# Performance work log

Hardware: AMD Instinct MI355X
Metric: run time of the kernel (lower is better)

Reference implementation:

```python
import jax, jax.numpy as jnp
import numpy as np

N = 50000   # nodes
E = 800000  # edges
IN, H, O, C = 128, 256, 256, 64
G = 64      # graphs in batch


def setup_inputs() -> dict:
    key = jax.random.key(0)
    ks = jax.random.split(key, 10)
    x = jax.random.normal(ks[0], (N, IN), dtype=jnp.float32)
    edge_index = jax.random.randint(ks[1], (2, E), 0, N, dtype=jnp.int32)
    batch = jnp.sort(jax.random.randint(ks[2], (N,), 0, G, dtype=jnp.int32))
    # learned params (PyG GCNConv: weight [in, out] + bias [out]; nn.Linear)
    W1 = jax.random.normal(ks[3], (IN, H), dtype=jnp.float32) / np.sqrt(IN)
    b1 = jnp.zeros((H,), dtype=jnp.float32)
    W2 = jax.random.normal(ks[4], (H, O), dtype=jnp.float32) / np.sqrt(H)
    b2 = jnp.zeros((O,), dtype=jnp.float32)
    Wfc = jax.random.normal(ks[5], (O, C), dtype=jnp.float32) / np.sqrt(O)
    bfc = jnp.zeros((C,), dtype=jnp.float32)
    return {"x": x, "edge_index": edge_index, "batch": batch,
            "W1": W1, "b1": b1, "W2": W2, "b2": b2, "Wfc": Wfc, "bfc": bfc}


def reference(x, edge_index, batch, W1, b1, W2, b2, Wfc, bfc):
    src, dst = edge_index[0], edge_index[1]
    # degree with self-loops (PyG GCNConv default: add_self_loops=True, sym norm)
    deg = jax.ops.segment_sum(jnp.ones((E,), x.dtype), dst, num_segments=N) + 1.0
    dinv = jax.lax.rsqrt(deg)                      # D^{-1/2}
    edge_norm = (dinv[src] * dinv[dst])[:, None]   # [E, 1]
    self_norm = (dinv * dinv)[:, None]             # [N, 1] self-loop weight

    def gcn_conv(h, W, b):
        h = h @ W                                  # transform first (PyG order)
        agg = jax.ops.segment_sum(h[src] * edge_norm, dst, num_segments=N)
        return agg + h * self_norm + b

    h = jax.nn.gelu(gcn_conv(x, W1, b1), approximate=False)  # nn.GELU exact
    h = gcn_conv(h, W2, b2)

    # global_mean_pool over graph ids
    cnt = jax.ops.segment_sum(jnp.ones((N,), h.dtype), batch, num_segments=G)
    pooled = jax.ops.segment_sum(h, batch, num_segments=G) / jnp.maximum(cnt, 1.0)[:, None]
    return pooled @ Wfc + bfc                      # [G, C]
```

## Files before the change

kernel.cpp:

```cpp
#include <hip/hip_runtime.h>
#include <hip/hip_bf16.h>
#include <hip/hip_fp16.h>
#include <math.h>

#define NNODES 50000
#define NEDGES 800000
#define FIN 128
#define FH 256
#define NG 64
#define NC 64
#define SCAN_NB ((NNODES + 255) / 256)
#define NP 50176
#define QSK 196
#define DEG_BLOCKS ((NEDGES + 255) / 256)
#define SPLITX_ITEMS (NNODES * FIN / 4)
#define SPLITX_BLOCKS ((SPLITX_ITEMS + 255) / 256)
#define WTZ_ITEMS (NG * NP / 4)
#define WTZ_BLOCKS ((WTZ_ITEMS + 255) / 256)
#define GEMM_MB ((NNODES + 127) / 128)
#define GEMM_BLKS (GEMM_MB * 2)
#define CVT_ITEMS (NG * NP / 4)
#define CVT_BLOCKS ((CVT_ITEMS + 255) / 256)

typedef unsigned short bhalf;
typedef __attribute__((ext_vector_type(8))) short bf16x8;
typedef __attribute__((ext_vector_type(4))) float f32x4;
typedef __attribute__((ext_vector_type(4))) unsigned short u16x4;

__device__ inline bhalf f2bf_rn(float f) {
    unsigned int u = __float_as_uint(f);
    u += 0x7FFFu + ((u >> 16) & 1u);
    return (bhalf)(u >> 16);
}
__device__ inline float bf2f(bhalf h) { return __uint_as_float(((unsigned int)h) << 16); }
__device__ inline float2 bfpair(unsigned int u) {
    return make_float2(__uint_as_float(u << 16), __uint_as_float(u & 0xFFFF0000u));
}
__device__ inline float edec_norm(unsigned int ed) {
    return __half2float(__ushort_as_half((unsigned short)(ed & 0xFFFFu)));
}


__global__ void degree_splitx_kernel(const int* __restrict__ dst, int* __restrict__ degi,
                                     int* __restrict__ rank, const float* __restrict__ x,
                                     bhalf* __restrict__ xb, float* __restrict__ wt) {
    int b = blockIdx.x;
    if (b < DEG_BLOCKS) {
        int e = b * 256 + threadIdx.x;
        if (e < NEDGES) rank[e] = atomicAdd(&degi[dst[e]], 1);
    } else if (b < DEG_BLOCKS + SPLITX_BLOCKS) {
        int i = (b - DEG_BLOCKS) * 256 + threadIdx.x;
        if (i < SPLITX_ITEMS) {
            float4 v = *reinterpret_cast<const float4*>(&x[i * 4]);
            u16x4 o = {f2bf_rn(v.x), f2bf_rn(v.y), f2bf_rn(v.z), f2bf_rn(v.w)};
            *reinterpret_cast<u16x4*>(&xb[i * 4]) = o;
        }
    } else {
        int i = (b - DEG_BLOCKS - SPLITX_BLOCKS) * 256 + threadIdx.x;
        if (i < WTZ_ITEMS) {
            f32x4 zr = {0.f, 0.f, 0.f, 0.f};
            *reinterpret_cast<f32x4*>(&wt[i * 4]) = zr;
        }
    }
}


__global__ __launch_bounds__(256)
void scan_block_kernel(const int* __restrict__ degi, int* __restrict__ local_ex,
                       int* __restrict__ partial, float* __restrict__ dinv, int Nn) {
    __shared__ int s[256];
    int i = blockIdx.x * 256 + threadIdx.x;
    int v = (i < Nn) ? degi[i] : 0;
    s[threadIdx.x] = v;
    __syncthreads();
#pragma unroll
    for (int off = 1; off < 256; off <<= 1) {
        int t = (threadIdx.x >= off) ? s[threadIdx.x - off] : 0;
        __syncthreads();
        s[threadIdx.x] += t;
        __syncthreads();
    }
    if (i < Nn) {
        local_ex[i] = s[threadIdx.x] - v;
        dinv[i] = rsqrtf((float)v + 1.0f);
    }
    if (threadIdx.x == 255) partial[blockIdx.x] = s[255];
}


__global__ __launch_bounds__(256)
void add_offsets_kernel(int* __restrict__ row_start, const int* __restrict__ local_ex,
                        const int* __restrict__ partial, const int* __restrict__ batch,
                        const float* __restrict__ dinv, float* __restrict__ wt,
                        const float* __restrict__ W1, bhalf* __restrict__ w1t, int Nn) {
    __shared__ int s[256];
    int t = threadIdx.x;
    s[t] = (t < blockIdx.x) ? partial[t] : 0;
    __syncthreads();
#pragma unroll
    for (int off = 128; off > 0; off >>= 1) {
        if (t < off) s[t] += s[t + off];
        __syncthreads();
    }
    int prefix = s[0];
    int i = blockIdx.x * 256 + t;
    if (i < Nn) {
        row_start[i] = local_ex[i] + prefix;
        float sn = dinv[i];
        atomicAdd(&wt[(size_t)batch[i] * NP + i], sn * sn);
    }
    if (i < FIN * 256) {
        int k = i >> 8, n = i & 255;
        w1t[n * FIN + k] = f2bf_rn(W1[i]);
    }
}


__global__ void edge_place_kernel(const int* __restrict__ src, const int* __restrict__ dst,
                                  const int* __restrict__ row_start, const int* __restrict__ rank,
                                  const float* __restrict__ dinv, const int* __restrict__ batch,
                                  unsigned int* __restrict__ edata, float* __restrict__ wt, int E) {
    int e = blockIdx.x * blockDim.x + threadIdx.x;
    if (e >= E) return;
    int s = src[e], d = dst[e];
    int pos = row_start[d] + rank[e];
    float nm = dinv[s] * dinv[d];
    unsigned short hb = __half_as_ushort(__float2half(nm));
    edata[pos] = ((unsigned int)s << 16) | (unsigned int)hb;
    atomicAdd(&wt[(size_t)batch[d] * NP + s], nm);
}


__global__ __launch_bounds__(256)
void gather128_kernel(const bhalf* __restrict__ xb, const unsigned int* __restrict__ edata,
                      const int* __restrict__ row_start, const int* __restrict__ degi,
                      const float* __restrict__ dinv, bhalf* __restrict__ z, int Nn) {
    int node = blockIdx.x * 4 + (threadIdx.x >> 6);
    if (node >= Nn) return;
    int lane = threadIdx.x & 63;
    int st = row_start[node];
    int cnt = degi[node];
    float ax = 0.0f, ay = 0.0f;
    int j = 0;
    for (; j + 3 < cnt; j += 4) {
        unsigned int e0 = edata[st + j],     e1 = edata[st + j + 1];
        unsigned int e2 = edata[st + j + 2], e3 = edata[st + j + 3];
        float2 v0 = bfpair(*reinterpret_cast<const unsigned int*>(&xb[(size_t)(e0 >> 16) * FIN + lane * 2]));
        float2 v1 = bfpair(*reinterpret_cast<const unsigned int*>(&xb[(size_t)(e1 >> 16) * FIN + lane * 2]));
        float2 v2 = bfpair(*reinterpret_cast<const unsigned int*>(&xb[(size_t)(e2 >> 16) * FIN + lane * 2]));
        float2 v3 = bfpair(*reinterpret_cast<const unsigned int*>(&xb[(size_t)(e3 >> 16) * FIN + lane * 2]));
        float n0 = edec_norm(e0), n1 = edec_norm(e1), n2 = edec_norm(e2), n3 = edec_norm(e3);
        ax += v0.x * n0 + v1.x * n1 + v2.x * n2 + v3.x * n3;
        ay += v0.y * n0 + v1.y * n1 + v2.y * n2 + v3.y * n3;
    }
    for (; j < cnt; j++) {
        unsigned int e0 = edata[st + j];
        float2 v0 = bfpair(*reinterpret_cast<const unsigned int*>(&xb[(size_t)(e0 >> 16) * FIN + lane * 2]));
        float n0 = edec_norm(e0);
        ax += v0.x * n0; ay += v0.y * n0;
    }
    float sn = dinv[node];
    sn *= sn;
    float2 xv = bfpair(*reinterpret_cast<const unsigned int*>(&xb[(size_t)node * FIN + lane * 2]));
    ushort2 o = {f2bf_rn(ax + xv.x * sn), f2bf_rn(ay + xv.y * sn)};
    *reinterpret_cast<ushort2*>(&z[(size_t)node * FIN + lane * 2]) = o;
}


__global__ __launch_bounds__(256)
void gemm_cvt_kernel(const bhalf* __restrict__ A, const bhalf* __restrict__ Bt,
                     const float* __restrict__ bias, bhalf* __restrict__ h1t,
                     const float* __restrict__ wt, bhalf* __restrict__ wthi,
                     bhalf* __restrict__ wtlo, int M, int Kp) {
    __shared__ bhalf As[128 * 72];
    __shared__ bhalf Bs[128 * 72];
    if (blockIdx.x >= GEMM_BLKS) {
        int i = (blockIdx.x - GEMM_BLKS) * 256 + threadIdx.x;
        if (i < CVT_ITEMS) {
            float4 v = *reinterpret_cast<const float4*>(&wt[i * 4]);
            u16x4 hi = {f2bf_rn(v.x), f2bf_rn(v.y), f2bf_rn(v.z), f2bf_rn(v.w)};
            u16x4 lo = {f2bf_rn(v.x - bf2f(hi.x)), f2bf_rn(v.y - bf2f(hi.y)),
                        f2bf_rn(v.z - bf2f(hi.z)), f2bf_rn(v.w - bf2f(hi.w))};
            *reinterpret_cast<u16x4*>(&wthi[i * 4]) = hi;
            *reinterpret_cast<u16x4*>(&wtlo[i * 4]) = lo;
        }
        return;
    }
    const int tid  = threadIdx.x;
    const int lane = tid & 63;
    const int wave = tid >> 6;
    const int quad = lane >> 4;
    const int l15  = lane & 15;
    const int wm = (wave & 1) * 64;
    const int wn = (wave >> 1) * 64;
    const int bm = (blockIdx.x >> 1) * 128;
    const int bn = (blockIdx.x & 1) * 128;

    f32x4 acc[4][4] = {};

    for (int k0 = 0; k0 < Kp; k0 += 64) {
#pragma unroll
        for (int i = 0; i < 4; i++) {
            int chunk = tid + i * 256;
            int r = chunk >> 3, c16 = chunk & 7;
            int gm = bm + r;
            float4 va = make_float4(0.f, 0.f, 0.f, 0.f);
            if (gm < M) va = *reinterpret_cast<const float4*>(&A[(size_t)gm * Kp + k0 + c16 * 8]);
            *reinterpret_cast<float4*>(&As[r * 72 + c16 * 8]) = va;
            float4 vb = *reinterpret_cast<const float4*>(&Bt[(size_t)(bn + r) * Kp + k0 + c16 * 8]);
            *reinterpret_cast<float4*>(&Bs[r * 72 + c16 * 8]) = vb;
        }
        __syncthreads();
#pragma unroll
        for (int kk = 0; kk < 64; kk += 32) {
            bf16x8 af[4], bfr[4];
#pragma unroll
            for (int mi = 0; mi < 4; mi++)
                af[mi] = *reinterpret_cast<const bf16x8*>(&As[(wm + mi * 16 + l15) * 72 + kk + quad * 8]);
#pragma unroll
            for (int ni = 0; ni < 4; ni++)
                bfr[ni] = *reinterpret_cast<const bf16x8*>(&Bs[(wn + ni * 16 + l15) * 72 + kk + quad * 8]);
#pragma unroll
            for (int mi = 0; mi < 4; mi++)
#pragma unroll
                for (int ni = 0; ni < 4; ni++)
                    acc[mi][ni] = __builtin_amdgcn_mfma_f32_16x16x32_bf16(af[mi], bfr[ni], acc[mi][ni], 0, 0, 0);
        }
        __syncthreads();
    }

#pragma unroll
    for (int mi = 0; mi < 4; mi++) {
        int row0 = bm + wm + mi * 16 + quad * 4;
#pragma unroll
        for (int ni = 0; ni < 4; ni++) {
            int col = bn + wn + ni * 16 + l15;
            float bv = bias[col];
            u16x4 o;
#pragma unroll
            for (int r = 0; r < 4; r++) {
                float v = acc[mi][ni][r] + bv;
                v = 0.5f * v * (1.0f + erff(v * 0.70710678118654752f));
                o[r] = f2bf_rn(v);
            }
            *reinterpret_cast<u16x4*>(&h1t[(size_t)col * NP + row0]) = o;
        }
    }
}


__global__ __launch_bounds__(256)
void qsum_mfma_kernel(const bhalf* __restrict__ h1t, const bhalf* __restrict__ wthi,
                      const bhalf* __restrict__ wtlo, float* __restrict__ qpart) {
    const int tid  = threadIdx.x;
    const int lane = tid & 63;
    const int wave = tid >> 6;
    const int quad = lane >> 4;
    const int l15  = lane & 15;
    const int m0 = wave * 64;
    const size_t kbase = (size_t)blockIdx.x * 256 + quad * 8;
    f32x4 acc[4][4] = {};
#pragma unroll
    for (int ks = 0; ks < 8; ks++) {
        size_t k0 = kbase + ks * 32;
        bf16x8 af[4], bh[4], bl[4];
#pragma unroll
        for (int mi = 0; mi < 4; mi++)
            af[mi] = *reinterpret_cast<const bf16x8*>(&h1t[(size_t)(m0 + mi * 16 + l15) * NP + k0]);
#pragma unroll
        for (int ni = 0; ni < 4; ni++) {
            bh[ni] = *reinterpret_cast<const bf16x8*>(&wthi[(size_t)(ni * 16 + l15) * NP + k0]);
            bl[ni] = *reinterpret_cast<const bf16x8*>(&wtlo[(size_t)(ni * 16 + l15) * NP + k0]);
        }
#pragma unroll
        for (int mi = 0; mi < 4; mi++)
#pragma unroll
            for (int ni = 0; ni < 4; ni++) {
                acc[mi][ni] = __builtin_amdgcn_mfma_f32_16x16x32_bf16(af[mi], bh[ni], acc[mi][ni], 0, 0, 0);
                acc[mi][ni] = __builtin_amdgcn_mfma_f32_16x16x32_bf16(af[mi], bl[ni], acc[mi][ni], 0, 0, 0);
            }
    }
    float* qp = &qpart[(size_t)blockIdx.x * NG * FH];
#pragma unroll
    for (int mi = 0; mi < 4; mi++) {
        int row0 = m0 + mi * 16 + quad * 4;
#pragma unroll
        for (int ni = 0; ni < 4; ni++) {
            int col = ni * 16 + l15;
            f32x4 o = {acc[mi][ni][0], acc[mi][ni][1], acc[mi][ni][2], acc[mi][ni][3]};
            *reinterpret_cast<f32x4*>(&qp[(size_t)col * FH + row0]) = o;
        }
    }
}


__global__ __launch_bounds__(256)
void p2fc_kernel(const float* __restrict__ qpart, const float* __restrict__ W2,
                 const float* __restrict__ b2, const int* __restrict__ batch,
                 const float* __restrict__ Wfc, const float* __restrict__ bfc,
                 float* __restrict__ out) {
    __shared__ float qg[FH];
    __shared__ float ps[FH];
    int g = blockIdx.x;
    int t = threadIdx.x;
    float s = 0.0f;
    for (int b = 0; b < QSK; b++)
        s += qpart[(size_t)b * NG * FH + (size_t)g * FH + t];
    qg[t] = s;
    int lo = 0, hi = NNODES;
    while (lo < hi) { int m = (lo + hi) >> 1; if (batch[m] < g) lo = m + 1; else hi = m; }
    int a = lo;
    lo = 0; hi = NNODES;
    while (lo < hi) { int m = (lo + hi) >> 1; if (batch[m] < g + 1) lo = m + 1; else hi = m; }
    float inv = 1.0f / fmaxf((float)(lo - a), 1.0f);
    __syncthreads();
    float acc = 0.0f;
    for (int k = 0; k < FH; k++)
        acc += qg[k] * W2[k * FH + t];
    ps[t] = acc * inv + b2[t];
    __syncthreads();
    if (t < NC) {
        float a2 = 0.0f;
        for (int cc = 0; cc < FH; cc++)
            a2 += ps[cc] * Wfc[cc * NC + t];
        out[g * NC + t] = a2 + bfc[t];
    }
}


extern "C" void kernel_launch(void* const* d_in, const int* in_sizes, int n_in,
                              void* d_out, int out_size, void* d_ws, size_t ws_size,
                              hipStream_t stream) {
    const float* x    = (const float*)d_in[0];
    const int*   ei   = (const int*)d_in[1];
    const int*   batch= (const int*)d_in[2];
    const float* W1   = (const float*)d_in[3];
    const float* b1   = (const float*)d_in[4];
    const float* W2   = (const float*)d_in[5];
    const float* b2   = (const float*)d_in[6];
    const float* Wfc  = (const float*)d_in[7];
    const float* bfc  = (const float*)d_in[8];
    float* out = (float*)d_out;

    const int* src = ei;
    const int* dst = ei + NEDGES;

    bhalf* xb        = (bhalf*)d_ws;
    bhalf* zb        = xb + (size_t)NNODES * FIN;
    bhalf* h1t       = zb + (size_t)NNODES * FIN;
    unsigned int* edata = (unsigned int*)(h1t + (size_t)FH * NP);
    int*   rank      = (int*)(edata + NEDGES);
    int*   row_start = rank + NEDGES;
    int*   local_ex  = row_start + NNODES;
    int*   partial   = local_ex + NNODES;
    float* dinv      = (float*)(partial + 256);
    bhalf* w1t       = (bhalf*)(dinv + NNODES);
    bhalf* wthi      = w1t + 256 * FIN;
    bhalf* wtlo      = wthi + (size_t)NG * NP;
    float* qpart     = (float*)(wtlo + (size_t)NG * NP);
    float* wt        = qpart + (size_t)QSK * NG * FH;
    int*   degi      = (int*)(wt + (size_t)NG * NP);

    (void)hipMemsetAsync(degi, 0, (size_t)NNODES * 4, stream);

    degree_splitx_kernel<<<DEG_BLOCKS + SPLITX_BLOCKS + WTZ_BLOCKS, 256, 0, stream>>>(
        dst, degi, rank, x, xb, wt);
    scan_block_kernel<<<SCAN_NB, 256, 0, stream>>>(degi, local_ex, partial, dinv, NNODES);
    add_offsets_kernel<<<SCAN_NB, 256, 0, stream>>>(row_start, local_ex, partial,
                                                    batch, dinv, wt, W1, w1t, NNODES);
    edge_place_kernel<<<(NEDGES + 255) / 256, 256, 0, stream>>>(src, dst, row_start, rank,
                                                                dinv, batch, edata, wt, NEDGES);

    gather128_kernel<<<(NNODES + 3) / 4, 256, 0, stream>>>(xb, edata, row_start, degi,
                                                           dinv, zb, NNODES);
    gemm_cvt_kernel<<<GEMM_BLKS + CVT_BLOCKS, 256, 0, stream>>>(zb, w1t, b1, h1t,
                                                                wt, wthi, wtlo, NNODES, FIN);

    qsum_mfma_kernel<<<QSK, 256, 0, stream>>>(h1t, wthi, wtlo, qpart);
    p2fc_kernel<<<NG, FH, 0, stream>>>(qpart, W2, b2, batch, Wfc, bfc, out);
}
```

Measured before the change: 275.9 us.

## Build pooled-weight matrix from CSR in shared memory instead of global atomics

Builds the per-graph pooling weight matrix wt with a new kernel. Each block owns one graph and a quarter of the node range, walks that graph's CSR edge range (found by binary search on the sorted batch array) and accumulates edge norms with shared-memory atomics. It then writes the bf16 hi/lo split directly. This removes the zeroing of the dense fp32 wt buffer, the global scattered atomics and the separate conversion pass. The edge record also changes from a packed 16-bit source plus fp16 norm to a uint2 holding a full source index and an fp32 norm, and per-edge rank atomics are replaced by a cursor atomic in edge placement. This doubles edge-list traffic in the gather and makes edge order within a row nondeterministic.

After: 302.2 us. 1.1x slower.

```diff
diff --git a/kernel.cpp b/kernel.cpp
--- a/kernel.cpp
+++ b/kernel.cpp
@@ -15,12 +15,9 @@
 #define DEG_BLOCKS ((NEDGES + 255) / 256)
 #define SPLITX_ITEMS (NNODES * FIN / 4)
 #define SPLITX_BLOCKS ((SPLITX_ITEMS + 255) / 256)
-#define WTZ_ITEMS (NG * NP / 4)
-#define WTZ_BLOCKS ((WTZ_ITEMS + 255) / 256)
 #define GEMM_MB ((NNODES + 127) / 128)
 #define GEMM_BLKS (GEMM_MB * 2)
-#define CVT_ITEMS (NG * NP / 4)
-#define CVT_BLOCKS ((CVT_ITEMS + 255) / 256)
+#define QTR (NP / 4)
 
 typedef unsigned short bhalf;
 typedef __attribute__((ext_vector_type(8))) short bf16x8;
@@ -36,30 +33,20 @@
 __device__ inline float2 bfpair(unsigned int u) {
     return make_float2(__uint_as_float(u << 16), __uint_as_float(u & 0xFFFF0000u));
 }
-__device__ inline float edec_norm(unsigned int ed) {
-    return __half2float(__ushort_as_half((unsigned short)(ed & 0xFFFFu)));
-}
 
 
 __global__ void degree_splitx_kernel(const int* __restrict__ dst, int* __restrict__ degi,
-                                     int* __restrict__ rank, const float* __restrict__ x,
-                                     bhalf* __restrict__ xb, float* __restrict__ wt) {
+                                     const float* __restrict__ x, bhalf* __restrict__ xb) {
     int b = blockIdx.x;
     if (b < DEG_BLOCKS) {
         int e = b * 256 + threadIdx.x;
-        if (e < NEDGES) rank[e] = atomicAdd(&degi[dst[e]], 1);
-    } else if (b < DEG_BLOCKS + SPLITX_BLOCKS) {
+        if (e < NEDGES) atomicAdd(&degi[dst[e]], 1);
+    } else {
         int i = (b - DEG_BLOCKS) * 256 + threadIdx.x;
         if (i < SPLITX_ITEMS) {
             float4 v = *reinterpret_cast<const float4*>(&x[i * 4]);
             u16x4 o = {f2bf_rn(v.x), f2bf_rn(v.y), f2bf_rn(v.z), f2bf_rn(v.w)};
             *reinterpret_cast<u16x4*>(&xb[i * 4]) = o;
-        }
-    } else {
-        int i = (b - DEG_BLOCKS - SPLITX_BLOCKS) * 256 + threadIdx.x;
-        if (i < WTZ_ITEMS) {
-            f32x4 zr = {0.f, 0.f, 0.f, 0.f};
-            *reinterpret_cast<f32x4*>(&wt[i * 4]) = zr;
         }
     }
 }
@@ -89,9 +76,8 @@
 
 
 __global__ __launch_bounds__(256)
-void add_offsets_kernel(int* __restrict__ row_start, const int* __restrict__ local_ex,
-                        const int* __restrict__ partial, const int* __restrict__ batch,
-                        const float* __restrict__ dinv, float* __restrict__ wt,
+void add_offsets_kernel(int* __restrict__ row_start, int* __restrict__ cursor,
+                        const int* __restrict__ local_ex, const int* __restrict__ partial,
                         const float* __restrict__ W1, bhalf* __restrict__ w1t, int Nn) {
     __shared__ int s[256];
     int t = threadIdx.x;
@@ -105,9 +91,9 @@
     int prefix = s[0];
     int i = blockIdx.x * 256 + t;
     if (i < Nn) {
-        row_start[i] = local_ex[i] + prefix;
-        float sn = dinv[i];
-        atomicAdd(&wt[(size_t)batch[i] * NP + i], sn * sn);
+        int rs = local_ex[i] + prefix;
+        row_start[i] = rs;
+        cursor[i] = rs;
     }
     if (i < FIN * 256) {
         int k = i >> 8, n = i & 255;
@@ -117,22 +103,19 @@
 
 
 __global__ void edge_place_kernel(const int* __restrict__ src, const int* __restrict__ dst,
-                                  const int* __restrict__ row_start, const int* __restrict__ rank,
-                                  const float* __restrict__ dinv, const int* __restrict__ batch,
-                                  unsigned int* __restrict__ edata, float* __restrict__ wt, int E) {
+                                  int* __restrict__ cursor, const float* __restrict__ dinv,
+                                  uint2* __restrict__ edata, int E) {
     int e = blockIdx.x * blockDim.x + threadIdx.x;
     if (e >= E) return;
     int s = src[e], d = dst[e];
-    int pos = row_start[d] + rank[e];
+    int pos = atomicAdd(&cursor[d], 1);
     float nm = dinv[s] * dinv[d];
-    unsigned short hb = __half_as_ushort(__float2half(nm));
-    edata[pos] = ((unsigned int)s << 16) | (unsigned int)hb;
-    atomicAdd(&wt[(size_t)batch[d] * NP + s], nm);
-}
-
-
-__global__ __launch_bounds__(256)
-void gather128_kernel(const bhalf* __restrict__ xb, const unsigned int* __restrict__ edata,
+    edata[pos] = make_uint2((unsigned int)s, __float_as_uint(nm));
+}
+
+
+__global__ __launch_bounds__(256)
+void gather128_kernel(const bhalf* __restrict__ xb, const uint2* __restrict__ edata,
                       const int* __restrict__ row_start, const int* __restrict__ degi,
                       const float* __restrict__ dinv, bhalf* __restrict__ z, int Nn) {
     int node = blockIdx.x * 4 + (threadIdx.x >> 6);
@@ -143,20 +126,21 @@
     float ax = 0.0f, ay = 0.0f;
     int j = 0;
     for (; j + 3 < cnt; j += 4) {
-        unsigned int e0 = edata[st + j],     e1 = edata[st + j + 1];
-        unsigned int e2 = edata[st + j + 2], e3 = edata[st + j + 3];
-        float2 v0 = bfpair(*reinterpret_cast<const unsigned int*>(&xb[(size_t)(e0 >> 16) * FIN + lane * 2]));
-        float2 v1 = bfpair(*reinterpret_cast<const unsigned int*>(&xb[(size_t)(e1 >> 16) * FIN + lane * 2]));
-        float2 v2 = bfpair(*reinterpret_cast<const unsigned int*>(&xb[(size_t)(e2 >> 16) * FIN + lane * 2]));
-        float2 v3 = bfpair(*reinterpret_cast<const unsigned int*>(&xb[(size_t)(e3 >> 16) * FIN + lane * 2]));
-        float n0 = edec_norm(e0), n1 = edec_norm(e1), n2 = edec_norm(e2), n3 = edec_norm(e3);
+        uint2 e0 = edata[st + j],     e1 = edata[st + j + 1];
+        uint2 e2 = edata[st + j + 2], e3 = edata[st + j + 3];
+        float2 v0 = bfpair(*reinterpret_cast<const unsigned int*>(&xb[(size_t)e0.x * FIN + lane * 2]));
+        float2 v1 = bfpair(*reinterpret_cast<const unsigned int*>(&xb[(size_t)e1.x * FIN + lane * 2]));
+        float2 v2 = bfpair(*reinterpret_cast<const unsigned int*>(&xb[(size_t)e2.x * FIN + lane * 2]));
+        float2 v3 = bfpair(*reinterpret_cast<const unsigned int*>(&xb[(size_t)e3.x * FIN + lane * 2]));
+        float n0 = __uint_as_float(e0.y), n1 = __uint_as_float(e1.y);
+        float n2 = __uint_as_float(e2.y), n3 = __uint_as_float(e3.y);
         ax += v0.x * n0 + v1.x * n1 + v2.x * n2 + v3.x * n3;
         ay += v0.y * n0 + v1.y * n1 + v2.y * n2 + v3.y * n3;
     }
     for (; j < cnt; j++) {
-        unsigned int e0 = edata[st + j];
-        float2 v0 = bfpair(*reinterpret_cast<const unsigned int*>(&xb[(size_t)(e0 >> 16) * FIN + lane * 2]));
-        float n0 = edec_norm(e0);
+        uint2 e0 = edata[st + j];
+        float2 v0 = bfpair(*reinterpret_cast<const unsigned int*>(&xb[(size_t)e0.x * FIN + lane * 2]));
+        float n0 = __uint_as_float(e0.y);
         ax += v0.x * n0; ay += v0.y * n0;
     }
     float sn = dinv[node];
@@ -168,24 +152,47 @@
 
 
 __global__ __launch_bounds__(256)
-void gemm_cvt_kernel(const bhalf* __restrict__ A, const bhalf* __restrict__ Bt,
-                     const float* __restrict__ bias, bhalf* __restrict__ h1t,
-                     const float* __restrict__ wt, bhalf* __restrict__ wthi,
-                     bhalf* __restrict__ wtlo, int M, int Kp) {
+void wt_build_kernel(const uint2* __restrict__ edata, const int* __restrict__ row_start,
+                     const int* __restrict__ batch, const float* __restrict__ dinv,
+                     bhalf* __restrict__ wthi, bhalf* __restrict__ wtlo) {
+    __shared__ float acc[QTR];
+    int g = blockIdx.x >> 2;
+    int q = blockIdx.x & 3;
+    int base = q * QTR;
+    for (int i = threadIdx.x; i < QTR; i += 256) acc[i] = 0.0f;
+    int lo = 0, hi = NNODES;
+    while (lo < hi) { int m = (lo + hi) >> 1; if (batch[m] < g) lo = m + 1; else hi = m; }
+    int na = lo;
+    hi = NNODES;
+    while (lo < hi) { int m = (lo + hi) >> 1; if (batch[m] < g + 1) lo = m + 1; else hi = m; }
+    int nb = lo;
+    int pa = (na < NNODES) ? row_start[na] : NEDGES;
+    int pb = (nb < NNODES) ? row_start[nb] : NEDGES;
+    __syncthreads();
+    for (int p = pa + threadIdx.x; p < pb; p += 256) {
+        uint2 e = edata[p];
+        int s = (int)e.x - base;
+        if ((unsigned int)s < (unsigned int)QTR)
+            atomicAdd(&acc[s], __uint_as_float(e.y));
+    }
+    __syncthreads();
+    size_t rowo = (size_t)g * NP + base;
+    for (int i = threadIdx.x; i < QTR; i += 256) {
+        int s = base + i;
+        float v = acc[i];
+        if (s >= na && s < nb) { float dv = dinv[s]; v += dv * dv; }
+        bhalf hb = f2bf_rn(v);
+        wthi[rowo + i] = hb;
+        wtlo[rowo + i] = f2bf_rn(v - bf2f(hb));
+    }
+}
+
+
+__global__ __launch_bounds__(256)
+void gemm_kernel(const bhalf* __restrict__ A, const bhalf* __restrict__ Bt,
+                 const float* __restrict__ bias, bhalf* __restrict__ h1t, int M, int Kp) {
     __shared__ bhalf As[128 * 72];
     __shared__ bhalf Bs[128 * 72];
-    if (blockIdx.x >= GEMM_BLKS) {
-        int i = (blockIdx.x - GEMM_BLKS) * 256 + threadIdx.x;
-        if (i < CVT_ITEMS) {
-            float4 v = *reinterpret_cast<const float4*>(&wt[i * 4]);
-            u16x4 hi = {f2bf_rn(v.x), f2bf_rn(v.y), f2bf_rn(v.z), f2bf_rn(v.w)};
-            u16x4 lo = {f2bf_rn(v.x - bf2f(hi.x)), f2bf_rn(v.y - bf2f(hi.y)),
-                        f2bf_rn(v.z - bf2f(hi.z)), f2bf_rn(v.w - bf2f(hi.w))};
-            *reinterpret_cast<u16x4*>(&wthi[i * 4]) = hi;
-            *reinterpret_cast<u16x4*>(&wtlo[i * 4]) = lo;
-        }
-        return;
-    }
     const int tid  = threadIdx.x;
     const int lane = tid & 63;
     const int wave = tid >> 6;
@@ -348,33 +355,31 @@
     bhalf* xb        = (bhalf*)d_ws;
     bhalf* zb        = xb + (size_t)NNODES * FIN;
     bhalf* h1t       = zb + (size_t)NNODES * FIN;
-    unsigned int* edata = (unsigned int*)(h1t + (size_t)FH * NP);
-    int*   rank      = (int*)(edata + NEDGES);
-    int*   row_start = rank + NEDGES;
-    int*   local_ex  = row_start + NNODES;
+    uint2* edata     = (uint2*)(h1t + (size_t)FH * NP);
+    int*   row_start = (int*)(edata + NEDGES);
+    int*   cursor    = row_start + NNODES;
+    int*   local_ex  = cursor + NNODES;
     int*   partial   = local_ex + NNODES;
     float* dinv      = (float*)(partial + 256);
     bhalf* w1t       = (bhalf*)(dinv + NNODES);
     bhalf* wthi      = w1t + 256 * FIN;
     bhalf* wtlo      = wthi + (size_t)NG * NP;
     float* qpart     = (float*)(wtlo + (size_t)NG * NP);
-    float* wt        = qpart + (size_t)QSK * NG * FH;
-    int*   degi      = (int*)(wt + (size_t)NG * NP);
+    int*   degi      = (int*)(qpart + (size_t)QSK * NG * FH);
 
     (void)hipMemsetAsync(degi, 0, (size_t)NNODES * 4, stream);
 
-    degree_splitx_kernel<<<DEG_BLOCKS + SPLITX_BLOCKS + WTZ_BLOCKS, 256, 0, stream>>>(
-        dst, degi, rank, x, xb, wt);
+    degree_splitx_kernel<<<DEG_BLOCKS + SPLITX_BLOCKS, 256, 0, stream>>>(dst, degi, x, xb);
     scan_block_kernel<<<SCAN_NB, 256, 0, stream>>>(degi, local_ex, partial, dinv, NNODES);
-    add_offsets_kernel<<<SCAN_NB, 256, 0, stream>>>(row_start, local_ex, partial,
-                                                    batch, dinv, wt, W1, w1t, NNODES);
-    edge_place_kernel<<<(NEDGES + 255) / 256, 256, 0, stream>>>(src, dst, row_start, rank,
-                                                                dinv, batch, edata, wt, NEDGES);
+    add_offsets_kernel<<<SCAN_NB, 256, 0, stream>>>(row_start, cursor, local_ex, partial,
+                                                    W1, w1t, NNODES);
+    edge_place_kernel<<<(NEDGES + 255) / 256, 256, 0, stream>>>(src, dst, cursor, dinv,
+                                                                edata, NEDGES);
 
     gather128_kernel<<<(NNODES + 3) / 4, 256, 0, stream>>>(xb, edata, row_start, degi,
                                                            dinv, zb, NNODES);
-    gemm_cvt_kernel<<<GEMM_BLKS + CVT_BLOCKS, 256, 0, stream>>>(zb, w1t, b1, h1t,
-                                                                wt, wthi, wtlo, NNODES, FIN);
+    wt_build_kernel<<<NG * 4, 256, 0, stream>>>(edata, row_start, batch, dinv, wthi, wtlo);
+    gemm_kernel<<<GEMM_BLKS, 256, 0, stream>>>(zb, w1t, b1, h1t, NNODES, FIN);
 
     qsum_mfma_kernel<<<QSK, 256, 0, stream>>>(h1t, wthi, wtlo, qpart);
     p2fc_kernel<<<NG, FH, 0, stream>>>(qpart, W2, b2, batch, Wfc, bfc, out);
```
